# Performance work log

Measured on AMD Instinct MI355X. Metric: run time of the kernel, lower is better.

## Reference

```python
import jax, jax.numpy as jnp
import numpy as np
from jax import lax

SD = 16          # sample_duration
STRIDE = 16      # feat_stride
SCALES = (4, 8, 16)
RATIOS = (0.5, 1.0, 2.0)
PRE_NMS = 1000   # proposals kept before NMS (TEST config)
POST_NMS = 128   # proposals kept after NMS
NMS_TH = 0.7


def _anchors2d():
    base = 16.0
    ctr = (base - 1.0) / 2.0
    out = []
    for r in RATIOS:
        ws = np.round(np.sqrt(base * base / r))
        hs = np.round(ws * r)
        for s in SCALES:
            w, h = ws * s, hs * s
            out.append([ctr - (w - 1) / 2, ctr - (h - 1) / 2,
                        ctr + (w - 1) / 2, ctr + (h - 1) / 2])
    return np.asarray(out, np.float32)                       # (9, 4)


def _anchors3d():
    # tube anchors: (x1, y1, t1, x2, y2, t2), durations [SD, SD/2, SD/4]
    a2 = _anchors2d()
    out = []
    for d in (SD, SD // 2, SD // 4):
        for a in a2:
            out.append([a[0], a[1], 0.0, a[2], a[3], d - 1.0])
    return np.asarray(out, np.float32)                       # (27, 6)


def _shifted(anchors, H, W):
    k = anchors.shape[-1]
    sx = jnp.arange(W, dtype=jnp.float32) * STRIDE
    sy = jnp.arange(H, dtype=jnp.float32) * STRIDE
    if k == 4:
        sh = jnp.stack(jnp.broadcast_arrays(sx[None, :], sy[:, None],
                                            sx[None, :], sy[:, None]), -1)
    else:
        z = jnp.zeros((H, W), jnp.float32)
        sh = jnp.stack(jnp.broadcast_arrays(sx[None, :], sy[:, None], z,
                                            sx[None, :], sy[:, None], z), -1)
    return (sh[:, :, None, :] + jnp.asarray(anchors)[None, None]).reshape(-1, k)


def _decode(anchors, deltas):
    # deltas layout: (d_ctr..., d_logsize...); works for 2D (k=4) and 3D (k=6)
    nd = anchors.shape[-1] // 2
    lo, hi = anchors[..., :nd], anchors[..., nd:]
    size = hi - lo + 1.0
    ctr = lo + 0.5 * (size - 1.0)
    pctr = deltas[..., :nd] * size + ctr
    psize = jnp.exp(deltas[..., nd:]) * size
    return jnp.concatenate([pctr - 0.5 * (psize - 1.0),
                            pctr + 0.5 * (psize - 1.0)], -1)


def _iou(b, boxes):
    # b: (k,), boxes: (N, k); area/volume IoU with +1 pixel convention
    nd = boxes.shape[-1] // 2
    lo = jnp.maximum(b[:nd], boxes[:, :nd])
    hi = jnp.minimum(b[nd:], boxes[:, nd:])
    inter = jnp.prod(jnp.maximum(hi - lo + 1.0, 0.0), -1)
    va = jnp.prod(b[nd:] - b[:nd] + 1.0)
    vb = jnp.prod(boxes[:, nd:] - boxes[:, :nd] + 1.0, -1)
    return inter / (va + vb - inter)


def _nms(boxes):
    # boxes already sorted by descending score; greedy NMS, fixed output size
    N = boxes.shape[0]

    def body(i, c):
        supp, keep = c
        idx = jnp.argmax(~supp)                 # first unsuppressed box
        keep = keep.at[i].set(idx.astype(jnp.int32))
        supp = supp | (_iou(boxes[idx], boxes) > NMS_TH)
        supp = supp.at[idx].set(True)
        return supp, keep

    _, keep = lax.fori_loop(0, POST_NMS, body,
                            (jnp.zeros(N, bool), jnp.zeros(POST_NMS, jnp.int32)))
    return keep


def _proposals(scores, deltas, anchors, maxs):
    # scores (B,N), deltas (B,N,k), anchors (N,k), maxs (B,1,k)
    boxes = jnp.clip(_decode(anchors[None], deltas), 0.0, maxs)
    _, idx = lax.top_k(scores, PRE_NMS)
    bx = jnp.take_along_axis(boxes, idx[..., None], axis=1)   # (B,PRE,k)
    keep = jax.vmap(_nms)(bx)                                 # (B,POST)
    sel = jnp.take_along_axis(bx, keep[..., None], axis=1)    # (B,POST,k)
    bidx = jnp.broadcast_to(
        jnp.arange(sel.shape[0], dtype=sel.dtype)[:, None, None],
        sel.shape[:2] + (1,))
    return lax.stop_gradient(jnp.concatenate([bidx, sel], -1))


def setup_inputs() -> dict:
    k = jax.random.split(jax.random.key(0), 8)
    s = 0.01
    return {
        "base_feat": jax.random.normal(k[0], (1, 256, 16, 32, 32), jnp.float32),
        "im_info": jnp.array([[512.0, 512.0, 1.0]], jnp.float32),
        "gt_boxes": jax.random.uniform(k[1], (1, 5, 7), jnp.float32) * 100.0,
        "gt_rois": jax.random.uniform(k[2], (1, 5, 16, 5), jnp.float32) * 100.0,
        "W_conv": jax.random.normal(k[3], (512, 256, 3, 3, 3), jnp.float32) * s,
        "b_conv": jnp.zeros((512,), jnp.float32),
        "W_cls": jax.random.normal(k[4], (54, 512), jnp.float32) * s,
        "b_cls": jnp.zeros((54,), jnp.float32),
        "W_bbox": jax.random.normal(k[5], (162, 512), jnp.float32) * s,
        "b_bbox": jnp.zeros((162,), jnp.float32),
        "W_cls16": jax.random.normal(k[6], (18, 512), jnp.float32) * s,
        "b_cls16": jnp.zeros((18,), jnp.float32),
        "W_bbox16": jax.random.normal(k[7], (36, 512), jnp.float32) * s,
        "b_bbox16": jnp.zeros((36,), jnp.float32),
    }


def reference(base_feat, im_info, gt_boxes, gt_rois, W_conv, b_conv,
              W_cls, b_cls, W_bbox, b_bbox, W_cls16, b_cls16,
              W_bbox16, b_bbox16):
    B, _, T, H, W = base_feat.shape
    # RPN_Conv: 3x3x3 Conv3d + ReLU
    conv1 = jax.nn.relu(
        lax.conv_general_dilated(base_feat, W_conv, (1, 1, 1), "SAME",
                                 dimension_numbers=("NCDHW", "OIDHW", "NCDHW"))
        + b_conv[None, :, None, None, None])
    # 1x1x1 score / bbox heads (3D)
    cls3 = jnp.einsum("bcthw,oc->bothw", conv1, W_cls) + b_cls[None, :, None, None, None]
    bbox3 = jnp.einsum("bcthw,oc->bothw", conv1, W_bbox) + b_bbox[None, :, None, None, None]
    # permute(0,1,3,4,2).mean(4) == mean over the temporal axis
    feat2 = conv1.mean(axis=2)
    cls2 = jnp.einsum("bchw,oc->bohw", feat2, W_cls16) + b_cls16[None, :, None, None]
    bbox2 = jnp.einsum("bchw,oc->bohw", feat2, W_bbox16) + b_bbox16[None, :, None, None]
    # reshape(x,2) + softmax over dim 1; fg prob is the second half of channels
    fg3 = jax.nn.softmax(cls3.reshape(B, 2, 27, T, H, W), axis=1)[:, 1]  # (B,27,T,H,W)
    fg2 = jax.nn.softmax(cls2.reshape(B, 2, 9, H, W), axis=1)[:, 1]      # (B,9,H,W)
    # proposal layers consume detached tensors (torch .data)
    fg3, fg2, bbox3d, bbox2d = map(lax.stop_gradient, (fg3, fg2, bbox3, bbox2))
    # flatten position-major (h, w, anchor)
    sc3 = fg3.mean(axis=2).transpose(0, 2, 3, 1).reshape(B, -1)
    dl3 = bbox3d.mean(axis=2).reshape(B, 27, 6, H, W).transpose(0, 3, 4, 1, 2).reshape(B, -1, 6)
    sc2 = fg2.transpose(0, 2, 3, 1).reshape(B, -1)
    dl2 = bbox2d.reshape(B, 9, 4, H, W).transpose(0, 3, 4, 1, 2).reshape(B, -1, 4)
    imh, imw = im_info[:, 0][:, None], im_info[:, 1][:, None]
    sdm = jnp.full_like(imw, SD - 1.0)
    max3 = jnp.stack([imw - 1, imh - 1, sdm, imw - 1, imh - 1, sdm], -1)  # (B,1,6)
    max2 = jnp.stack([imw - 1, imh - 1, imw - 1, imh - 1], -1)            # (B,1,4)
    rois = _proposals(sc3, dl3, _shifted(_anchors3d(), H, W), max3)       # (B,POST,7)
    rois16 = _proposals(sc2, dl2, _shifted(_anchors2d(), H, W), max2)     # (B,POST,5)
    z = jnp.zeros((), jnp.float32)  # eval mode: all RPN losses are 0
    return rois, rois16, z, z, z, z
```

## Files before the change

### kernel.cpp

```cpp
#include <hip/hip_runtime.h>
#include <hip/hip_bf16.h>
#include <cfloat>
#include <cstdint>


#define T_DIM 16
#define H_DIM 32
#define W_DIM 32
#define NVOX  (T_DIM*H_DIM*W_DIM)
#define HW    (H_DIM*W_DIM)
#define CIN   256
#define COUT  512
#define PRE_NMS 1000
#define POST_NMS 128
#define NMS_TH 0.7f

typedef __attribute__((ext_vector_type(8))) short v8s;
typedef __attribute__((ext_vector_type(4))) float v4f;
typedef __attribute__((ext_vector_type(4))) int v4i;

#define MFMA_B16(A,B,C) __builtin_amdgcn_mfma_f32_16x16x32_bf16(A,B,C,0,0,0)

__device__ __forceinline__ short f2bf(float x) {
    unsigned u = __float_as_uint(x);
    u += 0x7FFFu + ((u >> 16) & 1u);
    return (short)(u >> 16);
}
__device__ __forceinline__ float bf2f(short s) {
    return __uint_as_float(((unsigned)(unsigned short)s) << 16);
}

__constant__ float c_ws[3] = {23.f, 16.f, 11.f};
__constant__ float c_hs[3] = {12.f, 16.f, 22.f};
__constant__ float c_sc[3] = {4.f, 8.f, 16.f};
__constant__ float c_depth[3] = {16.f, 8.f, 4.f};

__global__ __launch_bounds__(256) void k_split_w(const float* __restrict__ W,
                                                 short* __restrict__ A0,
                                                 short* __restrict__ A1,
                                                 short* __restrict__ A2) {
    __shared__ float Wl[4][3456];
    const int b = blockIdx.x;
    const int t = threadIdx.x;
    const int og = b >> 1;
    const int ch = b & 1;
#pragma unroll
    for (int k = 0; k < 54; ++k) {
        int fi = t + k * 256;
        int ol = fi / 3456;
        int idx = fi - ol * 3456;
        Wl[ol][idx] = W[(size_t)(og * 4 + ol) * 6912 + ch * 3456 + idx];
    }
    __syncthreads();
    for (int p = t; p < 432; p += 256) {
        int tap = p >> 4, kol = p & 15;
        int ko = ch * 16 + kol;
        v8s vh[4], vm[4], vl[4];
#pragma unroll
        for (int ol = 0; ol < 4; ++ol)
#pragma unroll
            for (int c7 = 0; c7 < 8; ++c7) {
                float x = Wl[ol][(kol * 8 + c7) * 27 + tap];
                short hh = f2bf(x); float r = x - bf2f(hh);
                short mm = f2bf(r); float r2 = r - bf2f(mm);
                short ll = f2bf(r2);
                vh[ol][c7] = hh; vm[ol][c7] = mm; vl[ol][c7] = ll;
            }
        size_t base = ((size_t)(tap * 32 + ko) * 512 + og * 4) * 8;
#pragma unroll
        for (int q = 0; q < 4; ++q) {
            *(v8s*)(A0 + base + q * 8) = vh[q];
            *(v8s*)(A1 + base + q * 8) = vm[q];
            *(v8s*)(A2 + base + q * 8) = vl[q];
        }
    }
}

#define SPLIT2(X0, X1, OH, OM, OL) {                                          \
    unsigned u0_ = __float_as_uint(X0), u1_ = __float_as_uint(X1);            \
    OH = (int)__builtin_amdgcn_perm(u1_, u0_, 0x07060302u);                   \
    float h0_ = __uint_as_float(u0_ & 0xFFFF0000u);                           \
    float h1_ = __uint_as_float(u1_ & 0xFFFF0000u);                           \
    float r0_ = (X0) - h0_, r1_ = (X1) - h1_;                                 \
    unsigned v0_ = __float_as_uint(r0_), v1_ = __float_as_uint(r1_);          \
    OM = (int)__builtin_amdgcn_perm(v1_, v0_, 0x07060302u);                   \
    float m0_ = __uint_as_float(v0_ & 0xFFFF0000u);                           \
    float m1_ = __uint_as_float(v1_ & 0xFFFF0000u);                           \
    float s0_ = r0_ - m0_, s1_ = r1_ - m1_;                                   \
    OL = (int)__builtin_amdgcn_perm(__float_as_uint(s1_),                     \
                                    __float_as_uint(s0_), 0x07060302u);       \
}

__global__ void k_prep(const float* __restrict__ Wcls, const float* __restrict__ Wbb,
                       float* __restrict__ Wc, const float* __restrict__ I,
                       v4i* __restrict__ Ih, v4i* __restrict__ Im,
                       v4i* __restrict__ Il) {
    int blk = blockIdx.x;
    if (blk < 512) {
        int i = blk * 256 + threadIdx.x;
        int o = i & 255;
        int c = i >> 8;
        float v = 0.f;
        if (o < 54) v = Wcls[o * 512 + c];
        else if (o < 216) v = Wbb[(o - 54) * 512 + c];
        Wc[i] = v;
    } else {
        int t = (blk - 512) * 256 + threadIdx.x;
        int vox = t & 16383;
        int ck8 = t >> 14;
        const float* ip = I + ((size_t)ck8 << 3) * NVOX + vox;
        int h[4], m[4], l[4];
#pragma unroll
        for (int j = 0; j < 4; ++j) {
            float x0 = ip[(size_t)(2 * j) * NVOX];
            float x1 = ip[(size_t)(2 * j + 1) * NVOX];
            SPLIT2(x0, x1, h[j], m[j], l[j]);
        }
        Ih[t] = (v4i){h[0], h[1], h[2], h[3]};
        Im[t] = (v4i){m[0], m[1], m[2], m[3]};
        Il[t] = (v4i){l[0], l[1], l[2], l[3]};
    }
}

#define CV_SHIFT(TAP) {                                                       \
    int kt_ = (TAP) / 9 - 1, kh_ = ((TAP) / 3) % 3 - 1, kw_ = (TAP) % 3 - 1;  \
    int tt_ = bt + kt_, hh_ = bh + kh_, ww_ = bw + kw_;                       \
    bVal = ((unsigned)tt_ < 16u) && ((unsigned)hh_ < 32u) && ((unsigned)ww_ < 32u); \
    bOff = bVal ? ((tt_ << 10) + (hh_ << 5) + ww_) : 0;                       \
}

#define CV_LOAD_BP(CK8B) {                                                    \
    const size_t bidx_ = (((size_t)((CK8B) + skh * 2)) << 14) + bOff;         \
    nh0 = Ih[bidx_]; nh1 = Ih[bidx_ + NVOX];                                  \
    nm0 = Im[bidx_]; nm1 = Im[bidx_ + NVOX];                                  \
    nl0 = Il[bidx_]; nl1 = Il[bidx_ + NVOX];                                  \
}

#define LOAD_ASET_M(S, H0,H1,H2,H3, M0,M1,M2,M3, L0,L1,L2,L3) {               \
    const size_t aB_ = (((size_t)((S) >> 3) * 32 + (((S) & 7) << 2)) << 12) + aLane; \
    H0 = *(const v8s*)(A0 + aB_);       H1 = *(const v8s*)(A0 + aB_ + 128);   \
    H2 = *(const v8s*)(A0 + aB_ + 256); H3 = *(const v8s*)(A0 + aB_ + 384);   \
    M0 = *(const v8s*)(A1 + aB_);       M1 = *(const v8s*)(A1 + aB_ + 128);   \
    M2 = *(const v8s*)(A1 + aB_ + 256); M3 = *(const v8s*)(A1 + aB_ + 384);   \
    L0 = *(const v8s*)(A2 + aB_);       L1 = *(const v8s*)(A2 + aB_ + 128);   \
    L2 = *(const v8s*)(A2 + aB_ + 256); L3 = *(const v8s*)(A2 + aB_ + 384);   \
}

#define COMPUTE_M(BUF, H0,H1,H2,H3, M0,M1,M2,M3, L0,L1,L2,L3) {               \
    _Pragma("unroll")                                                         \
    for (int j = 0; j < 4; ++j) {                                             \
        v8s bb = *(const v8s*)(&Bsh[BUF][0][uB + j * 16]);                    \
        v8s bm = *(const v8s*)(&Bsh[BUF][1][uB + j * 16]);                    \
        v8s bl = *(const v8s*)(&Bsh[BUF][2][uB + j * 16]);                    \
        v4f a;                                                                \
        a = acc[0][j];                                                        \
        a = MFMA_B16(H0, bb, a); a = MFMA_B16(H0, bm, a);                     \
        a = MFMA_B16(M0, bb, a); a = MFMA_B16(H0, bl, a);                     \
        a = MFMA_B16(M0, bm, a); a = MFMA_B16(L0, bb, a);                     \
        acc[0][j] = a;                                                        \
        a = acc[1][j];                                                        \
        a = MFMA_B16(H1, bb, a); a = MFMA_B16(H1, bm, a);                     \
        a = MFMA_B16(M1, bb, a); a = MFMA_B16(H1, bl, a);                     \
        a = MFMA_B16(M1, bm, a); a = MFMA_B16(L1, bb, a);                     \
        acc[1][j] = a;                                                        \
        a = acc[2][j];                                                        \
        a = MFMA_B16(H2, bb, a); a = MFMA_B16(H2, bm, a);                     \
        a = MFMA_B16(M2, bb, a); a = MFMA_B16(H2, bl, a);                     \
        a = MFMA_B16(M2, bm, a); a = MFMA_B16(L2, bb, a);                     \
        acc[2][j] = a;                                                        \
        a = acc[3][j];                                                        \
        a = MFMA_B16(H3, bb, a); a = MFMA_B16(H3, bm, a);                     \
        a = MFMA_B16(M3, bb, a); a = MFMA_B16(H3, bl, a);                     \
        a = MFMA_B16(M3, bm, a); a = MFMA_B16(L3, bb, a);                     \
        acc[3][j] = a;                                                        \
    }                                                                         \
}

#define LOAD_ASET(S, ...) LOAD_ASET_M(S, __VA_ARGS__)
#define COMPUTE(BUF, ...) COMPUTE_M(BUF, __VA_ARGS__)

#define ASET(P) P##h0,P##h1,P##h2,P##h3,P##m0,P##m1,P##m2,P##m3,P##l0,P##l1,P##l2,P##l3

#define ITER_BODY(SS, BUF, CUR, ALT) {                                        \
    int s1_ = (SS) + 1, s2_ = (SS) + 2;                                       \
    if (s1_ < 216) { LOAD_ASET(s1_, ASET(ALT)); }                             \
    if (s1_ < 216) {                                                          \
        v4i z_ = (v4i){0, 0, 0, 0};                                           \
        Bsh[(BUF) ^ 1][0][uW0] = bValCur ? nh0 : z_;                          \
        Bsh[(BUF) ^ 1][0][uW1] = bValCur ? nh1 : z_;                          \
        Bsh[(BUF) ^ 1][1][uW0] = bValCur ? nm0 : z_;                          \
        Bsh[(BUF) ^ 1][1][uW1] = bValCur ? nm1 : z_;                          \
        Bsh[(BUF) ^ 1][2][uW0] = bValCur ? nl0 : z_;                          \
        Bsh[(BUF) ^ 1][2][uW1] = bValCur ? nl1 : z_;                          \
    }                                                                         \
    if (s2_ < 216) {                                                          \
        if ((s2_ & 7) == 0) CV_SHIFT(s2_ >> 3);                               \
        CV_LOAD_BP((s2_ & 7) << 2);                                           \
        bValCur = bVal;                                                       \
    }                                                                         \
    COMPUTE(BUF, ASET(CUR));                                                  \
}

#define BAR_LDS() { asm volatile("s_waitcnt lgkmcnt(0)" ::: "memory");        \
                    __builtin_amdgcn_s_barrier(); }

__global__ __launch_bounds__(256, 2) void k_conv3d_mfma(
        const v4i* __restrict__ Ih, const v4i* __restrict__ Im,
        const v4i* __restrict__ Il, const short* __restrict__ A0,
        const short* __restrict__ A1, const short* __restrict__ A2,
        const float* __restrict__ bias, float* __restrict__ O) {
    __shared__ v4i Bsh[2][3][512];
    const int tid = threadIdx.x;
    const int o0 = blockIdx.y * 128;
    const int v0 = blockIdx.x * 128;
    const int lane = tid & 63;
    const int wv = tid >> 6;
    const int quad = lane >> 4, m16 = lane & 15;
    const int wo = (wv >> 1) * 64;
    const int wvx = (wv & 1) * 64;

    const int sa_o = tid >> 1, skh = tid & 1;
    const int uW0 = (skh * 2) * 128 + sa_o;
    const int uW1 = (skh * 2 + 1) * 128 + sa_o;

    const int vbase = v0 + sa_o;
    const int bt = vbase >> 10, bh = (vbase >> 5) & 31, bw = vbase & 31;

    const int uB = quad * 128 + wvx + m16;

    const size_t aLane = ((size_t)(o0 + wo + m16) << 3) + ((size_t)quad << 12);

    v4f acc[4][4];
#pragma unroll
    for (int i = 0; i < 4; i++)
#pragma unroll
        for (int j = 0; j < 4; j++) acc[i][j] = (v4f){0.f, 0.f, 0.f, 0.f};

    int bOff, bVal, bValCur;
    v4i nh0, nh1, nm0, nm1, nl0, nl1;
    v8s Ph0, Ph1, Ph2, Ph3, Pm0, Pm1, Pm2, Pm3, Pl0, Pl1, Pl2, Pl3;
    v8s Qh0, Qh1, Qh2, Qh3, Qm0, Qm1, Qm2, Qm3, Ql0, Ql1, Ql2, Ql3;

    CV_SHIFT(0);
    bValCur = bVal;
    CV_LOAD_BP(0);
    {
        v4i z_ = (v4i){0, 0, 0, 0};
        Bsh[0][0][uW0] = bValCur ? nh0 : z_;
        Bsh[0][0][uW1] = bValCur ? nh1 : z_;
        Bsh[0][1][uW0] = bValCur ? nm0 : z_;
        Bsh[0][1][uW1] = bValCur ? nm1 : z_;
        Bsh[0][2][uW0] = bValCur ? nl0 : z_;
        Bsh[0][2][uW1] = bValCur ? nl1 : z_;
    }
    CV_LOAD_BP(4);
    LOAD_ASET(0, ASET(P));
    __syncthreads();

    for (int s = 0; s < 216; s += 2) {
        ITER_BODY(s, 0, P, Q);
        BAR_LDS();
        ITER_BODY(s + 1, 1, Q, P);
        BAR_LDS();
    }

#pragma unroll
    for (int i = 0; i < 4; ++i) {
#pragma unroll
        for (int r = 0; r < 4; ++r) {
            int o = o0 + wo + i * 16 + quad * 4 + r;
            float bo = bias[o];
            float* dst = O + (size_t)o * NVOX + v0 + wvx + m16;
#pragma unroll
            for (int j = 0; j < 4; ++j)
                dst[j * 16] = fmaxf(acc[i][j][r] + bo, 0.f);
        }
    }
}

__global__ __launch_bounds__(256) void k_gemm_logits3(const float* __restrict__ conv1,
                                                      const float* __restrict__ Wc,
                                                      float* __restrict__ L) {
    __shared__ float As[16][64];
    __shared__ float Bs[16][64];
    const int tid = threadIdx.x;
    const int o0 = blockIdx.y * 64;
    const int v0 = blockIdx.x * 64;
    const int ty = tid >> 4, tx = tid & 15;
    const int c_l = tid >> 4, e4 = (tid & 15) << 2;

    float acc[4][4];
#pragma unroll
    for (int i = 0; i < 4; i++)
#pragma unroll
        for (int j = 0; j < 4; j++) acc[i][j] = 0.f;

    for (int ck = 0; ck < 512; ck += 16) {
        __syncthreads();
        *(float4*)(&As[c_l][e4]) = *(const float4*)(Wc + ((size_t)(ck + c_l) << 8) + o0 + e4);
        *(float4*)(&Bs[c_l][e4]) = *(const float4*)(conv1 + ((size_t)(ck + c_l) << 14) + v0 + e4);
        __syncthreads();
#pragma unroll
        for (int k = 0; k < 16; ++k) {
            float a[4], b[4];
            *(float4*)(a) = *(const float4*)(&As[k][ty * 4]);
            *(float4*)(b) = *(const float4*)(&Bs[k][tx * 4]);
#pragma unroll
            for (int i = 0; i < 4; i++)
#pragma unroll
                for (int j = 0; j < 4; j++)
                    acc[i][j] = fmaf(a[i], b[j], acc[i][j]);
        }
    }
#pragma unroll
    for (int i = 0; i < 4; i++) {
        float* dst = L + (size_t)(o0 + ty * 4 + i) * NVOX + v0 + tx * 4;
        *(float4*)(dst) = *(const float4*)(&acc[i][0]);
    }
}

__global__ void k_heads3(const float* __restrict__ L, const float* __restrict__ b_cls,
                         const float* __restrict__ b_bbox, const float* __restrict__ conv1,
                         float* __restrict__ sc3, float* __restrict__ dl3,
                         float* __restrict__ feat2) {
    int i = blockIdx.x * 256 + threadIdx.x;
    if (i < 27 * HW) {
        int a = i >> 10, hw = i & 1023;
        float b0 = b_cls[a], b1 = b_cls[27 + a];
        const float* L0 = L + (size_t)a * NVOX + hw;
        const float* L1 = L + (size_t)(27 + a) * NVOX + hw;
        float s = 0.f;
        for (int t = 0; t < T_DIM; t++) {
            float x0 = L0[t * HW] + b0, x1 = L1[t * HW] + b1;
            float m = fmaxf(x0, x1);
            float e0 = expf(x0 - m), e1 = expf(x1 - m);
            s += e1 / (e0 + e1);
        }
        sc3[hw * 27 + a] = s * (1.f / 16.f);
    } else if (i < (27 + 162) * HW) {
        int ii = i - 27 * HW;
        int ch = ii >> 10, hw = ii & 1023;
        const float* Lr = L + (size_t)(54 + ch) * NVOX + hw;
        float s = 0.f;
        for (int t = 0; t < T_DIM; t++) s += Lr[t * HW];
        s = s * (1.f / 16.f) + b_bbox[ch];
        int a = ch / 6, d = ch - a * 6;
        dl3[((size_t)hw * 27 + a) * 6 + d] = s;
    } else {
        int ii = i - (27 + 162) * HW;
        int c = ii >> 10, hw = ii & 1023;
        const float* src = conv1 + (size_t)c * NVOX + hw;
        float s = 0.f;
        for (int t = 0; t < T_DIM; t++) s += src[t * HW];
        feat2[ii] = s * (1.f / 16.f);
    }
}

__global__ void k_gemm2d(const float* __restrict__ feat2, const float* __restrict__ Wcls16,
                         const float* __restrict__ Wbb16, float* __restrict__ L2) {
    int g = blockIdx.x * 256 + threadIdx.x;
    int o = g >> 10, hw = g & 1023;
    const float* wrow = (o < 18) ? (Wcls16 + (size_t)o * 512) : (Wbb16 + (size_t)(o - 18) * 512);
    float s = 0.f;
    for (int c = 0; c < 512; c++) s = fmaf(wrow[c], feat2[(size_t)c * HW + hw], s);
    L2[(size_t)o * HW + hw] = s;
}

__global__ void k_heads2(const float* __restrict__ L2, const float* __restrict__ b_cls16,
                         const float* __restrict__ b_bbox16,
                         float* __restrict__ sc2, float* __restrict__ dl2) {
    int i = blockIdx.x * 256 + threadIdx.x;
    if (i < 9 * HW) {
        int a = i >> 10, hw = i & 1023;
        float x0 = L2[(size_t)a * HW + hw] + b_cls16[a];
        float x1 = L2[(size_t)(9 + a) * HW + hw] + b_cls16[9 + a];
        float m = fmaxf(x0, x1);
        float e0 = expf(x0 - m), e1 = expf(x1 - m);
        sc2[hw * 9 + a] = e1 / (e0 + e1);
    } else if (i < 45 * HW) {
        int ii = i - 9 * HW;
        int ch = ii >> 10, hw = ii & 1023;
        float v = L2[(size_t)(18 + ch) * HW + hw] + b_bbox16[ch];
        int a = ch >> 2, d = ch & 3;
        dl2[((size_t)hw * 9 + a) * 4 + d] = v;
    }
}

__device__ __forceinline__ unsigned mapf(float f) {
    unsigned u = __float_as_uint(f);
    return (u & 0x80000000u) ? ~u : (u | 0x80000000u);
}

__global__ __launch_bounds__(1024) void k_propA(const float* __restrict__ im_info,
                                                const float* __restrict__ sc3,
                                                const float* __restrict__ dl3,
                                                const float* __restrict__ sc2,
                                                const float* __restrict__ dl2,
                                                float* __restrict__ bxg) {
    const int branch = blockIdx.x;
    const int tid = threadIdx.x;
    const int A = (branch == 0) ? 27 : 9;
    const int nd = (branch == 0) ? 3 : 2;
    const float* scores = (branch == 0) ? sc3 : sc2;
    const float* deltas = (branch == 0) ? dl3 : dl2;
    const int K = PRE_NMS;
    const int ept = A;
    const int base = tid * ept;

    __shared__ unsigned hist[256];
    __shared__ unsigned long long keys[1024];
    __shared__ unsigned wsum[16];
    __shared__ int sh_b, sh_next;

    unsigned prefix = 0;
    int rank = K;
    for (int shift = 24; shift >= 0; shift -= 8) {
        if (tid < 256) hist[tid] = 0;
        __syncthreads();
        const unsigned mask_hi = (shift == 24) ? 0u : (0xFFFFFFFFu << (shift + 8));
        for (int j = 0; j < ept; j++) {
            unsigned m = mapf(scores[base + j]);
            if ((m & mask_hi) == prefix)
                atomicAdd(&hist[(m >> shift) & 255], 1u);
        }
        __syncthreads();
        for (int d = 1; d < 256; d <<= 1) {
            unsigned add = 0;
            if (tid < 256 && tid + d < 256) add = hist[tid + d];
            __syncthreads();
            if (tid < 256) hist[tid] += add;
            __syncthreads();
        }
        if (tid < 256) {
            bool win = (hist[tid] >= (unsigned)rank) &&
                       (tid == 255 || hist[tid + 1] < (unsigned)rank);
            if (win) { sh_b = tid; sh_next = (tid == 255) ? 0 : (int)hist[tid + 1]; }
        }
        __syncthreads();
        prefix |= (unsigned)sh_b << shift;
        rank -= sh_next;
        __syncthreads();
    }
    const unsigned tau = prefix;

    int gt_c = 0, eq_c = 0;
    for (int j = 0; j < ept; j++) {
        unsigned m = mapf(scores[base + j]);
        gt_c += (m > tau);
        eq_c += (m == tau);
    }
    unsigned cnt = ((unsigned)gt_c << 16) | (unsigned)eq_c;
    const int lane = tid & 63, wid = tid >> 6;
    unsigned x = cnt;
    for (int d = 1; d < 64; d <<= 1) {
        unsigned y = __shfl_up(x, d);
        if (lane >= d) x += y;
    }
    if (lane == 63) wsum[wid] = x;
    __syncthreads();
    if (wid == 0) {
        unsigned w = (lane < 16) ? wsum[lane] : 0;
        for (int d = 1; d < 16; d <<= 1) {
            unsigned y = __shfl_up(w, d);
            if (lane >= d) w += y;
        }
        if (lane < 16) wsum[lane] = w;
    }
    __syncthreads();
    unsigned excl = x - cnt + (wid ? wsum[wid - 1] : 0);
    const int c1 = (int)(wsum[15] >> 16);
    int gi = (int)(excl >> 16);
    int ei = (int)(excl & 0xFFFFu);
    for (int j = 0; j < ept; j++) {
        int idx = base + j;
        unsigned m = mapf(scores[idx]);
        unsigned long long key = ((unsigned long long)m << 32) |
                                 (unsigned)(0xFFFFFFFFu - (unsigned)idx);
        if (m > tau) {
            keys[gi++] = key;
        } else if (m == tau) {
            if (c1 + ei < K) keys[c1 + ei] = key;
            ei++;
        }
    }
    if (tid < 1024 - K) keys[K + tid] = 0;
    __syncthreads();

    for (int k = 2; k <= 1024; k <<= 1) {
        for (int j = k >> 1; j > 0; j >>= 1) {
            int ixj = tid ^ j;
            if (ixj > tid) {
                unsigned long long a = keys[tid], b = keys[ixj];
                bool sw2 = ((tid & k) == 0) ? (a < b) : (a > b);
                if (sw2) { keys[tid] = b; keys[ixj] = a; }
            }
            __syncthreads();
        }
    }

    const float imh = im_info[0], imw = im_info[1];
    if (tid < K) {
        int n = (int)(0xFFFFFFFFu - (unsigned)(keys[tid] & 0xFFFFFFFFull));
        int cell = n / A, a = n - cell * A;
        int hc = cell >> 5, wc = cell & 31;
        int a2 = (branch == 0) ? (a % 9) : a;
        int ri = a2 / 3, si = a2 % 3;
        float w = c_ws[ri] * c_sc[si], h = c_hs[ri] * c_sc[si];
        float lo[3], hi[3], mx[3];
        lo[0] = 7.5f - (w - 1.f) * 0.5f + 16.f * wc;
        hi[0] = 7.5f + (w - 1.f) * 0.5f + 16.f * wc;
        mx[0] = imw - 1.f;
        lo[1] = 7.5f - (h - 1.f) * 0.5f + 16.f * hc;
        hi[1] = 7.5f + (h - 1.f) * 0.5f + 16.f * hc;
        mx[1] = imh - 1.f;
        if (branch == 0) { lo[2] = 0.f; hi[2] = c_depth[a / 9] - 1.f; mx[2] = (float)(T_DIM - 1); }
        const float* dp = deltas + (size_t)n * (2 * nd);
        float* bp = bxg + ((size_t)branch * PRE_NMS + tid) * 6;
        for (int d = 0; d < nd; d++) {
            float size = hi[d] - lo[d] + 1.f;
            float ctr = lo[d] + 0.5f * (size - 1.f);
            float pctr = dp[d] * size + ctr;
            float psize = expf(dp[nd + d]) * size;
            float pl = pctr - 0.5f * (psize - 1.f);
            float ph = pctr + 0.5f * (psize - 1.f);
            bp[d]      = fminf(fmaxf(pl, 0.f), mx[d]);
            bp[nd + d] = fminf(fmaxf(ph, 0.f), mx[d]);
        }
    }
}

__global__ __launch_bounds__(256) void k_iou(const float* __restrict__ bxg,
                                             unsigned long long* __restrict__ masks) {
    int g = blockIdx.x * 256 + threadIdx.x;
    if (g >= 2 * PRE_NMS * 16) return;
    int branch = g / (PRE_NMS * 16);
    int rem = g - branch * (PRE_NMS * 16);
    int r = rem >> 4, w = rem & 15;
    int nd = (branch == 0) ? 3 : 2;
    const float* B = bxg + (size_t)branch * PRE_NMS * 6;
    float rb[6];
#pragma unroll
    for (int d = 0; d < 6; d++) rb[d] = B[(size_t)r * 6 + d];
    unsigned long long mword = 0;
    int c0 = w * 64;
    for (int j = 0; j < 64; ++j) {
        int c = c0 + j;
        if (c >= PRE_NMS) break;
        const float* cb = B + (size_t)c * 6;
        float colvol = 1.f;
        for (int d = 0; d < nd; d++) colvol *= (cb[nd + d] - cb[d] + 1.f);
        float inter = 1.f, rvol = 1.f;
        for (int d = 0; d < nd; d++) {
            float slo = rb[d], shi = rb[nd + d];
            float l = fmaxf(slo, cb[d]);
            float hh = fminf(shi, cb[nd + d]);
            inter *= fmaxf(hh - l + 1.f, 0.f);
            rvol *= (shi - slo + 1.f);
        }
        float iou = inter / (rvol + colvol - inter);
        if ((iou > NMS_TH) || (c == r)) mword |= (1ull << j);
    }
    masks[((size_t)branch * PRE_NMS + r) * 16 + w] = mword;
}

__global__ __launch_bounds__(64) void k_nms(const unsigned long long* __restrict__ masks,
                                            const float* __restrict__ bxg,
                                            float* __restrict__ out) {
    const int branch = blockIdx.x;
    const int lane = threadIdx.x;
    const unsigned long long* M = masks + (size_t)branch * PRE_NMS * 16;
    __shared__ int keep[POST_NMS];
    unsigned long long alive = 0;
    if (lane < 15) alive = ~0ull;
    else if (lane == 15) alive = (1ull << (PRE_NMS - 15 * 64)) - 1;
    for (int i = 0; i < POST_NMS; ++i) {
        int cand = (lane < 16 && alive) ? (lane * 64 + __ffsll(alive) - 1) : 0x7fffffff;
#pragma unroll
        for (int off = 32; off; off >>= 1)
            cand = min(cand, __shfl_xor(cand, off));
        int sel = (cand == 0x7fffffff) ? 0 : cand;
        if (lane == 0) keep[i] = sel;
        if (lane < 16) alive &= ~M[(size_t)sel * 16 + lane];
    }
    __syncthreads();
    const float* B = bxg + (size_t)branch * PRE_NMS * 6;
    for (int e = lane; e < POST_NMS; e += 64) {
        int k = keep[e];
        if (branch == 0) {
            float* o = out + (size_t)e * 7;
            o[0] = 0.f;
            for (int d = 0; d < 6; d++) o[1 + d] = B[(size_t)k * 6 + d];
        } else {
            float* o = out + 128 * 7 + (size_t)e * 5;
            o[0] = 0.f;
            for (int d = 0; d < 4; d++) o[1 + d] = B[(size_t)k * 6 + d];
        }
    }
    if (branch == 0 && lane == 0) {
        out[1536] = 0.f; out[1537] = 0.f; out[1538] = 0.f; out[1539] = 0.f;
    }
}

extern "C" void kernel_launch(void* const* d_in, const int* in_sizes, int n_in,
                              void* d_out, int out_size, void* d_ws, size_t ws_size,
                              hipStream_t stream) {
    (void)in_sizes; (void)n_in; (void)out_size; (void)ws_size;
    const float* base_feat = (const float*)d_in[0];
    const float* im_info   = (const float*)d_in[1];
    const float* W_conv    = (const float*)d_in[4];
    const float* b_conv    = (const float*)d_in[5];
    const float* W_cls     = (const float*)d_in[6];
    const float* b_cls     = (const float*)d_in[7];
    const float* W_bbox    = (const float*)d_in[8];
    const float* b_bbox    = (const float*)d_in[9];
    const float* W_cls16   = (const float*)d_in[10];
    const float* b_cls16   = (const float*)d_in[11];
    const float* W_bbox16  = (const float*)d_in[12];
    const float* b_bbox16  = (const float*)d_in[13];
    float* out = (float*)d_out;

    char* ws = (char*)d_ws;
    const size_t AW = (size_t)27 * 512 * 256;
    short* A0 = (short*)ws;
    short* A1 = A0 + AW;
    short* A2 = A1 + AW;
    float* L3 = (float*)ws;
    size_t off = AW * 3 * sizeof(short);
    float* Wcomb  = (float*)(ws + off); off += (size_t)512 * 256 * 4;
    float* conv1  = (float*)(ws + off); off += (size_t)COUT * NVOX * 4;
    float* feat2  = (float*)(ws + off); off += (size_t)512 * HW * 4;
    float* L2     = (float*)(ws + off); off += (size_t)64 * HW * 4;
    float* sc3    = (float*)(ws + off); off += (size_t)27 * HW * 4;
    float* dl3    = (float*)(ws + off); off += (size_t)27 * HW * 6 * 4;
    float* sc2    = (float*)(ws + off); off += (size_t)9 * HW * 4;
    float* dl2    = (float*)(ws + off); off += (size_t)9 * HW * 4 * 4;
    v4i* Ih = (v4i*)(ws + off); off += (size_t)32 * NVOX * 16;
    v4i* Im_ = (v4i*)(ws + off); off += (size_t)32 * NVOX * 16;
    v4i* Il = (v4i*)(ws + off); off += (size_t)32 * NVOX * 16;
    float* bxg = (float*)(ws + off); off += (size_t)2 * PRE_NMS * 6 * 4;
    unsigned long long* masks = (unsigned long long*)(ws + off);
    off += (size_t)2 * PRE_NMS * 16 * 8;

    k_split_w<<<256, 256, 0, stream>>>(W_conv, A0, A1, A2);
    k_prep<<<512 + 2048, 256, 0, stream>>>(W_cls, W_bbox, Wcomb, base_feat, Ih, Im_, Il);
    {
        dim3 g(NVOX / 128, COUT / 128);
        k_conv3d_mfma<<<g, 256, 0, stream>>>(Ih, Im_, Il, A0, A1, A2, b_conv, conv1);
    }
    {
        dim3 g(NVOX / 64, 4);
        k_gemm_logits3<<<g, 256, 0, stream>>>(conv1, Wcomb, L3);
    }
    k_heads3<<<(27 + 162 + 512) * HW / 256, 256, 0, stream>>>(L3, b_cls, b_bbox, conv1,
                                                              sc3, dl3, feat2);
    k_gemm2d<<<(54 * HW) / 256, 256, 0, stream>>>(feat2, W_cls16, W_bbox16, L2);
    k_heads2<<<(45 * HW) / 256, 256, 0, stream>>>(L2, b_cls16, b_bbox16, sc2, dl2);
    k_propA<<<2, 1024, 0, stream>>>(im_info, sc3, dl3, sc2, dl2, bxg);
    k_iou<<<(2 * PRE_NMS * 16 + 255) / 256, 256, 0, stream>>>(bxg, masks);
    k_nms<<<2, 64, 0, stream>>>(masks, bxg, out);
}
```

Baseline: 935.1 us.

## Halve conv output tile and single-buffer LDS to raise occupancy

The MFMA conv3d kernel's output-channel tile drops from 128 to 64 per block, so each wave keeps 2x4 accumulators instead of 4x4 and holds half as many A fragments. The LDS B buffer goes from double to single buffering, with two barriers per step, and launch bounds are raised to 4 blocks per CU. The aim is to cut register and LDS pressure so more waves can hide memory latency. In exchange, B-tile data is reused half as much per load, global B traffic doubles because twice as many blocks load the same voxels, and the extra barrier per step exposes LDS write latency.

```diff
diff --git a/kernel.cpp b/kernel.cpp
--- a/kernel.cpp
+++ b/kernel.cpp
@@ -136,22 +136,19 @@
     nl0 = Il[bidx_]; nl1 = Il[bidx_ + NVOX];                                  \
 }
 
-#define LOAD_ASET_M(S, H0,H1,H2,H3, M0,M1,M2,M3, L0,L1,L2,L3) {               \
+#define LOAD_ASET_M(S, H0,H1, M0,M1, L0,L1) {                                 \
     const size_t aB_ = (((size_t)((S) >> 3) * 32 + (((S) & 7) << 2)) << 12) + aLane; \
-    H0 = *(const v8s*)(A0 + aB_);       H1 = *(const v8s*)(A0 + aB_ + 128);   \
-    H2 = *(const v8s*)(A0 + aB_ + 256); H3 = *(const v8s*)(A0 + aB_ + 384);   \
-    M0 = *(const v8s*)(A1 + aB_);       M1 = *(const v8s*)(A1 + aB_ + 128);   \
-    M2 = *(const v8s*)(A1 + aB_ + 256); M3 = *(const v8s*)(A1 + aB_ + 384);   \
-    L0 = *(const v8s*)(A2 + aB_);       L1 = *(const v8s*)(A2 + aB_ + 128);   \
-    L2 = *(const v8s*)(A2 + aB_ + 256); L3 = *(const v8s*)(A2 + aB_ + 384);   \
-}
-
-#define COMPUTE_M(BUF, H0,H1,H2,H3, M0,M1,M2,M3, L0,L1,L2,L3) {               \
+    H0 = *(const v8s*)(A0 + aB_); H1 = *(const v8s*)(A0 + aB_ + 128);         \
+    M0 = *(const v8s*)(A1 + aB_); M1 = *(const v8s*)(A1 + aB_ + 128);         \
+    L0 = *(const v8s*)(A2 + aB_); L1 = *(const v8s*)(A2 + aB_ + 128);         \
+}
+
+#define COMPUTE_M(H0,H1, M0,M1, L0,L1) {                                      \
     _Pragma("unroll")                                                         \
     for (int j = 0; j < 4; ++j) {                                             \
-        v8s bb = *(const v8s*)(&Bsh[BUF][0][uB + j * 16]);                    \
-        v8s bm = *(const v8s*)(&Bsh[BUF][1][uB + j * 16]);                    \
-        v8s bl = *(const v8s*)(&Bsh[BUF][2][uB + j * 16]);                    \
+        v8s bb = *(const v8s*)(&Bsh[0][uB + j * 16]);                         \
+        v8s bm = *(const v8s*)(&Bsh[1][uB + j * 16]);                         \
+        v8s bl = *(const v8s*)(&Bsh[2][uB + j * 16]);                         \
         v4f a;                                                                \
         a = acc[0][j];                                                        \
         a = MFMA_B16(H0, bb, a); a = MFMA_B16(H0, bm, a);                     \
@@ -163,60 +160,54 @@
         a = MFMA_B16(M1, bb, a); a = MFMA_B16(H1, bl, a);                     \
         a = MFMA_B16(M1, bm, a); a = MFMA_B16(L1, bb, a);                     \
         acc[1][j] = a;                                                        \
-        a = acc[2][j];                                                        \
-        a = MFMA_B16(H2, bb, a); a = MFMA_B16(H2, bm, a);                     \
-        a = MFMA_B16(M2, bb, a); a = MFMA_B16(H2, bl, a);                     \
-        a = MFMA_B16(M2, bm, a); a = MFMA_B16(L2, bb, a);                     \
-        acc[2][j] = a;                                                        \
-        a = acc[3][j];                                                        \
-        a = MFMA_B16(H3, bb, a); a = MFMA_B16(H3, bm, a);                     \
-        a = MFMA_B16(M3, bb, a); a = MFMA_B16(H3, bl, a);                     \
-        a = MFMA_B16(M3, bm, a); a = MFMA_B16(L3, bb, a);                     \
-        acc[3][j] = a;                                                        \
     }                                                                         \
 }
 
 #define LOAD_ASET(S, ...) LOAD_ASET_M(S, __VA_ARGS__)
-#define COMPUTE(BUF, ...) COMPUTE_M(BUF, __VA_ARGS__)
-
-#define ASET(P) P##h0,P##h1,P##h2,P##h3,P##m0,P##m1,P##m2,P##m3,P##l0,P##l1,P##l2,P##l3
-
-#define ITER_BODY(SS, BUF, CUR, ALT) {                                        \
-    int s1_ = (SS) + 1, s2_ = (SS) + 2;                                       \
-    if (s1_ < 216) { LOAD_ASET(s1_, ASET(ALT)); }                             \
-    if (s1_ < 216) {                                                          \
-        v4i z_ = (v4i){0, 0, 0, 0};                                           \
-        Bsh[(BUF) ^ 1][0][uW0] = bValCur ? nh0 : z_;                          \
-        Bsh[(BUF) ^ 1][0][uW1] = bValCur ? nh1 : z_;                          \
-        Bsh[(BUF) ^ 1][1][uW0] = bValCur ? nm0 : z_;                          \
-        Bsh[(BUF) ^ 1][1][uW1] = bValCur ? nm1 : z_;                          \
-        Bsh[(BUF) ^ 1][2][uW0] = bValCur ? nl0 : z_;                          \
-        Bsh[(BUF) ^ 1][2][uW1] = bValCur ? nl1 : z_;                          \
-    }                                                                         \
-    if (s2_ < 216) {                                                          \
-        if ((s2_ & 7) == 0) CV_SHIFT(s2_ >> 3);                               \
-        CV_LOAD_BP((s2_ & 7) << 2);                                           \
-        bValCur = bVal;                                                       \
-    }                                                                         \
-    COMPUTE(BUF, ASET(CUR));                                                  \
-}
+#define COMPUTE(...) COMPUTE_M(__VA_ARGS__)
+
+#define ASET(P) P##h0,P##h1,P##m0,P##m1,P##l0,P##l1
 
 #define BAR_LDS() { asm volatile("s_waitcnt lgkmcnt(0)" ::: "memory");        \
                     __builtin_amdgcn_s_barrier(); }
 
-__global__ __launch_bounds__(256, 2) void k_conv3d_mfma(
+#define ITER1(SS, CUR, ALT) {                                                 \
+    BAR_LDS();                                                                \
+    {                                                                         \
+        v4i z_ = (v4i){0, 0, 0, 0};                                           \
+        Bsh[0][uW0] = bValCur ? nh0 : z_;                                     \
+        Bsh[0][uW1] = bValCur ? nh1 : z_;                                     \
+        Bsh[1][uW0] = bValCur ? nm0 : z_;                                     \
+        Bsh[1][uW1] = bValCur ? nm1 : z_;                                     \
+        Bsh[2][uW0] = bValCur ? nl0 : z_;                                     \
+        Bsh[2][uW1] = bValCur ? nl1 : z_;                                     \
+    }                                                                         \
+    BAR_LDS();                                                                \
+    {                                                                         \
+        int s1_ = (SS) + 1;                                                   \
+        if (s1_ < 216) {                                                      \
+            if ((s1_ & 7) == 0) CV_SHIFT(s1_ >> 3);                           \
+            CV_LOAD_BP((s1_ & 7) << 2);                                       \
+            bValCur = bVal;                                                   \
+            LOAD_ASET(s1_, ASET(ALT));                                        \
+        }                                                                     \
+    }                                                                         \
+    COMPUTE(ASET(CUR));                                                       \
+}
+
+__global__ __launch_bounds__(256, 4) void k_conv3d_mfma(
         const v4i* __restrict__ Ih, const v4i* __restrict__ Im,
         const v4i* __restrict__ Il, const short* __restrict__ A0,
         const short* __restrict__ A1, const short* __restrict__ A2,
         const float* __restrict__ bias, float* __restrict__ O) {
-    __shared__ v4i Bsh[2][3][512];
+    __shared__ v4i Bsh[3][512];
     const int tid = threadIdx.x;
-    const int o0 = blockIdx.y * 128;
+    const int o0 = blockIdx.y * 64;
     const int v0 = blockIdx.x * 128;
     const int lane = tid & 63;
     const int wv = tid >> 6;
     const int quad = lane >> 4, m16 = lane & 15;
-    const int wo = (wv >> 1) * 64;
+    const int wo = (wv >> 1) * 32;
     const int wvx = (wv & 1) * 64;
 
     const int sa_o = tid >> 1, skh = tid & 1;
@@ -230,42 +221,29 @@
 
     const size_t aLane = ((size_t)(o0 + wo + m16) << 3) + ((size_t)quad << 12);
 
-    v4f acc[4][4];
-#pragma unroll
-    for (int i = 0; i < 4; i++)
+    v4f acc[2][4];
+#pragma unroll
+    for (int i = 0; i < 2; i++)
 #pragma unroll
         for (int j = 0; j < 4; j++) acc[i][j] = (v4f){0.f, 0.f, 0.f, 0.f};
 
     int bOff, bVal, bValCur;
     v4i nh0, nh1, nm0, nm1, nl0, nl1;
-    v8s Ph0, Ph1, Ph2, Ph3, Pm0, Pm1, Pm2, Pm3, Pl0, Pl1, Pl2, Pl3;
-    v8s Qh0, Qh1, Qh2, Qh3, Qm0, Qm1, Qm2, Qm3, Ql0, Ql1, Ql2, Ql3;
+    v8s Ph0, Ph1, Pm0, Pm1, Pl0, Pl1;
+    v8s Qh0, Qh1, Qm0, Qm1, Ql0, Ql1;
 
     CV_SHIFT(0);
     bValCur = bVal;
     CV_LOAD_BP(0);
-    {
-        v4i z_ = (v4i){0, 0, 0, 0};
-        Bsh[0][0][uW0] = bValCur ? nh0 : z_;
-        Bsh[0][0][uW1] = bValCur ? nh1 : z_;
-        Bsh[0][1][uW0] = bValCur ? nm0 : z_;
-        Bsh[0][1][uW1] = bValCur ? nm1 : z_;
-        Bsh[0][2][uW0] = bValCur ? nl0 : z_;
-        Bsh[0][2][uW1] = bValCur ? nl1 : z_;
-    }
-    CV_LOAD_BP(4);
     LOAD_ASET(0, ASET(P));
-    __syncthreads();
 
     for (int s = 0; s < 216; s += 2) {
-        ITER_BODY(s, 0, P, Q);
-        BAR_LDS();
-        ITER_BODY(s + 1, 1, Q, P);
-        BAR_LDS();
-    }
-
-#pragma unroll
-    for (int i = 0; i < 4; ++i) {
+        ITER1(s, P, Q);
+        ITER1(s + 1, Q, P);
+    }
+
+#pragma unroll
+    for (int i = 0; i < 2; ++i) {
 #pragma unroll
         for (int r = 0; r < 4; ++r) {
             int o = o0 + wo + i * 16 + quad * 4 + r;
@@ -644,7 +622,7 @@
     k_split_w<<<256, 256, 0, stream>>>(W_conv, A0, A1, A2);
     k_prep<<<512 + 2048, 256, 0, stream>>>(W_cls, W_bbox, Wcomb, base_feat, Ih, Im_, Il);
     {
-        dim3 g(NVOX / 128, COUT / 128);
+        dim3 g(NVOX / 128, COUT / 64);
         k_conv3d_mfma<<<g, 256, 0, stream>>>(Ih, Im_, Il, A0, A1, A2, b_conv, conv1);
     }
     {
```

After: 1.076 ms. 15.1% more time.
